# Kernel tuning notes

Hardware: AMD Instinct MI355X
Metric: run time of the kernel (lower is better)

The kernel has to match this reference:

```python
import jax, jax.numpy as jnp
import numpy as np

EPS = 0.01      # label smoothing eps
LAM = 0.5       # SuperLoss lam
ALPHA = 0.25    # FocalLoss alpha
GAMMA = 2.0     # FocalLoss gamma


def lambertw_principal(y, iters=20):
    """Real principal-branch Lambert W for y >= -1/e, via Halley iterations.
    Replaces the scipy.special.lambertw CPU round-trip with on-device math."""
    y = jnp.maximum(y, -jnp.exp(-1.0) + 1e-7)  # clamp to domain of W0
    # init: branch-point series near -1/e, log1p-based elsewhere
    p = jnp.sqrt(2.0 * (jnp.e * y + 1.0))
    w_bp = -1.0 + p - p * p / 3.0
    w = jnp.where(y < 0.0, w_bp, jnp.log1p(y))

    def body(w, _):
        ew = jnp.exp(w)
        f = w * ew - y
        w1 = w + 1.0
        w_next = w - f / (ew * w1 - (w + 2.0) * f / (2.0 * w1))
        return w_next, None

    w, _ = jax.lax.scan(body, w, None, length=iters)
    return w


def setup_inputs() -> dict:
    key = jax.random.key(0)
    k1, k2 = jax.random.split(key)
    B, C = 2048, 50257
    output = jax.random.normal(k1, (B, C), dtype=jnp.float32)
    target = jax.random.randint(k2, (B,), 0, C, dtype=jnp.int64)
    return {"output": output, "target": target}


def reference(output, target):
    B, c = output.shape
    # label-smoothing uniform term: mean over batch of -sum(log_softmax)
    log_preds = jax.nn.log_softmax(output, axis=-1)          # [B, C]
    loss = (-log_preds.sum(axis=-1)).mean()                  # scalar

    # FocalLoss(Superloss=True) applied to log_preds (CE re-applies log_softmax,
    # idempotent on log_preds but kept for fidelity)
    lp2 = jax.nn.log_softmax(log_preds, axis=-1)
    ce = -jnp.take_along_axis(lp2, target[:, None], axis=-1)[:, 0]  # [B]
    pt = jnp.exp(-ce)
    focal = ALPHA * (1.0 - pt) ** GAMMA * ce                 # [B]

    # SuperLoss: sigma computed from detached loss (stop_gradient)
    tau = jnp.log(jnp.float32(c))                            # C == classes
    l_det = jax.lax.stop_gradient(focal)
    cl_score = l_det - tau
    y_ = 0.5 * jnp.maximum(-2.0 / jnp.e, cl_score / LAM)
    sigma = jnp.exp(-lambertw_principal(y_))                 # [B]
    sl = (focal - tau) * sigma + LAM * jnp.log(sigma) ** 2
    sl_mean = sl.mean()

    loss_cls = loss * EPS / c + (1.0 - EPS) * sl_mean
    return loss_cls, jnp.exp(sl_mean)
```

## Files before the change

kernel.cpp:

```cpp
#include <hip/hip_runtime.h>
#include <hip/hip_bf16.h>
#include <math.h>


#define EPS_LS 0.01
#define LAM 0.5
#define ALPHA 0.25

__global__ __launch_bounds__(256) void
row_kernel(const float* __restrict__ x, const int* __restrict__ tgt,
           double* __restrict__ ws, int B, int C) {
    const int row = blockIdx.x;
    const int tid = threadIdx.x;
    const float* xr = x + (size_t)row * (size_t)C;

    float m  = -3.402823466e38f;
    float s  = 0.0f;
    float sx = 0.0f;

    const int mis = (int)(((size_t)row * (size_t)C) & 3);
    const int pre = (4 - mis) & 3;
    if (tid < pre) {
        float v = xr[tid];
        m = v; s = 1.0f; sx = v;
    }
    const int nvec = (C - pre) >> 2;
    const float4* xv = reinterpret_cast<const float4*>(xr + pre);
    for (int i = tid; i < nvec; i += 256) {
        float4 v = xv[i];
        float mx = fmaxf(fmaxf(v.x, v.y), fmaxf(v.z, v.w));
        float nm = fmaxf(m, mx);
        s = s * __expf(m - nm)
          + __expf(v.x - nm) + __expf(v.y - nm)
          + __expf(v.z - nm) + __expf(v.w - nm);
        m = nm;
        sx += (v.x + v.y) + (v.z + v.w);
    }
    const int done = pre + (nvec << 2);
    const int rem = C - done;
    if (tid < rem) {
        float v = xr[done + tid];
        float nm = fmaxf(m, v);
        s = s * __expf(m - nm) + __expf(v - nm);
        m = nm;
        sx += v;
    }

    for (int off = 32; off > 0; off >>= 1) {
        float mo  = __shfl_down(m, off, 64);
        float so  = __shfl_down(s, off, 64);
        float sxo = __shfl_down(sx, off, 64);
        float nm = fmaxf(m, mo);
        s = s * __expf(m - nm) + so * __expf(mo - nm);
        m = nm;
        sx += sxo;
    }

    __shared__ float sh_m[4], sh_s[4], sh_sx[4];
    const int wave = tid >> 6, lane = tid & 63;
    if (lane == 0) { sh_m[wave] = m; sh_s[wave] = s; sh_sx[wave] = sx; }
    __syncthreads();

    if (tid == 0) {
        float M = sh_m[0], S = sh_s[0], SX = sh_sx[0];
        for (int wv = 1; wv < 4; ++wv) {
            float nm = fmaxf(M, sh_m[wv]);
            S = S * __expf(M - nm) + sh_s[wv] * __expf(sh_m[wv] - nm);
            M = nm;
            SX += sh_sx[wv];
        }
        const double lse = log((double)S);
        const double xt  = (double)xr[tgt[row]];
        const double ce  = (double)M + lse - xt;
        const double pt  = exp(-ce);
        const double omp = 1.0 - pt;
        const double focal = ALPHA * omp * omp * ce;
        const double tau = log((double)C);
        const double cl  = focal - tau;
        const double Econst = 2.718281828459045235360287;
        double y_ = 0.5 * fmax(-2.0 / Econst, cl / LAM);
        double y  = fmax(y_, -exp(-1.0) + 1e-7);
        double p  = sqrt(2.0 * (Econst * y + 1.0));
        double w  = (y < 0.0) ? (-1.0 + p - p * p / 3.0) : log1p(y);
        for (int it = 0; it < 20; ++it) {
            double ew = exp(w);
            double f  = w * ew - y;
            double w1 = w + 1.0;
            w = w - f / (ew * w1 - (w + 2.0) * f / (2.0 * w1));
        }
        const double sigma = exp(-w);
        const double lw = log(sigma);
        const double sl = cl * sigma + LAM * lw * lw;
        const double rowloss = (double)C * ((double)M + lse) - (double)SX;
        ws[row]     = sl;
        ws[B + row] = rowloss;
    }
}

__global__ __launch_bounds__(256) void
finalize_kernel(const double* __restrict__ ws, float* __restrict__ out,
                int B, int C) {
    __shared__ double shA[256], shB[256];
    const int tid = threadIdx.x;
    double a = 0.0, b = 0.0;
    for (int i = tid; i < B; i += 256) {
        a += ws[i];
        b += ws[B + i];
    }
    shA[tid] = a; shB[tid] = b;
    __syncthreads();
    for (int off = 128; off > 0; off >>= 1) {
        if (tid < off) { shA[tid] += shA[tid + off]; shB[tid] += shB[tid + off]; }
        __syncthreads();
    }
    if (tid == 0) {
        const double sl_mean = shA[0] / (double)B;
        const double loss    = shB[0] / (double)B;
        const double loss_cls = loss * (EPS_LS / (double)C) + (1.0 - EPS_LS) * sl_mean;
        out[0] = (float)loss_cls;
        out[1] = (float)exp(sl_mean);
    }
}

extern "C" void kernel_launch(void* const* d_in, const int* in_sizes, int n_in,
                              void* d_out, int out_size, void* d_ws, size_t ws_size,
                              hipStream_t stream) {
    const float* x   = (const float*)d_in[0];
    const int*   tgt = (const int*)d_in[1];
    float* out = (float*)d_out;
    double* ws = (double*)d_ws;

    const int B = in_sizes[1];
    const int C = in_sizes[0] / B;

    row_kernel<<<B, 256, 0, stream>>>(x, tgt, ws, B, C);
    finalize_kernel<<<1, 256, 0, stream>>>(ws, out, B, C);
}
```

Baseline: 543.0 us.

## Unroll row scan with dual accumulators and nontemporal loads, move scalar math to finalize

The row kernel now issues two independent vector loads per iteration with nontemporal hints, keeps two online-softmax accumulators and merges them at the end. This is meant to raise memory-level parallelism and cut streaming cache pollution. The per-row double-precision focal and Lambert-W work moves from thread 0 of each row block into the single-block finalize kernel, which shortens the tail of each row block. The cost is that finalize now runs this serial double math for 8 rows per thread on one workgroup and gathers target logits from global memory.

```diff
diff --git a/kernel.cpp b/kernel.cpp
--- a/kernel.cpp
+++ b/kernel.cpp
@@ -7,77 +7,107 @@
 #define LAM 0.5
 #define ALPHA 0.25
 
+typedef float vf4 __attribute__((ext_vector_type(4)));
+
+struct Acc { float m, s, sx; };
+
+__device__ __forceinline__ void acc_vec(Acc& a, vf4 v) {
+    float mx = fmaxf(fmaxf(v.x, v.y), fmaxf(v.z, v.w));
+    float nm = fmaxf(a.m, mx);
+    a.s = a.s * __expf(a.m - nm)
+        + __expf(v.x - nm) + __expf(v.y - nm)
+        + __expf(v.z - nm) + __expf(v.w - nm);
+    a.m = nm;
+    a.sx += (v.x + v.y) + (v.z + v.w);
+}
+
+__device__ __forceinline__ void acc_merge(Acc& a, float mo, float so, float sxo) {
+    float nm = fmaxf(a.m, mo);
+    a.s = a.s * __expf(a.m - nm) + so * __expf(mo - nm);
+    a.m = nm;
+    a.sx += sxo;
+}
+
 __global__ __launch_bounds__(256) void
-row_kernel(const float* __restrict__ x, const int* __restrict__ tgt,
-           double* __restrict__ ws, int B, int C) {
+row_kernel(const float* __restrict__ x, float4* __restrict__ ws, int C) {
     const int row = blockIdx.x;
     const int tid = threadIdx.x;
     const float* xr = x + (size_t)row * (size_t)C;
 
-    float m  = -3.402823466e38f;
-    float s  = 0.0f;
-    float sx = 0.0f;
+    Acc a0 = { -3.402823466e38f, 0.0f, 0.0f };
+    Acc a1 = { -3.402823466e38f, 0.0f, 0.0f };
 
     const int mis = (int)(((size_t)row * (size_t)C) & 3);
     const int pre = (4 - mis) & 3;
     if (tid < pre) {
         float v = xr[tid];
-        m = v; s = 1.0f; sx = v;
+        a0.m = v; a0.s = 1.0f; a0.sx = v;
     }
     const int nvec = (C - pre) >> 2;
-    const float4* xv = reinterpret_cast<const float4*>(xr + pre);
-    for (int i = tid; i < nvec; i += 256) {
-        float4 v = xv[i];
-        float mx = fmaxf(fmaxf(v.x, v.y), fmaxf(v.z, v.w));
-        float nm = fmaxf(m, mx);
-        s = s * __expf(m - nm)
-          + __expf(v.x - nm) + __expf(v.y - nm)
-          + __expf(v.z - nm) + __expf(v.w - nm);
-        m = nm;
-        sx += (v.x + v.y) + (v.z + v.w);
+    const vf4* xv = reinterpret_cast<const vf4*>(xr + pre);
+
+    int i = tid;
+    for (; i + 256 < nvec; i += 512) {
+        vf4 v0 = __builtin_nontemporal_load(&xv[i]);
+        vf4 v1 = __builtin_nontemporal_load(&xv[i + 256]);
+        acc_vec(a0, v0);
+        acc_vec(a1, v1);
+    }
+    if (i < nvec) {
+        vf4 v0 = __builtin_nontemporal_load(&xv[i]);
+        acc_vec(a0, v0);
     }
     const int done = pre + (nvec << 2);
     const int rem = C - done;
     if (tid < rem) {
         float v = xr[done + tid];
-        float nm = fmaxf(m, v);
-        s = s * __expf(m - nm) + __expf(v - nm);
-        m = nm;
-        sx += v;
+        float nm = fmaxf(a0.m, v);
+        a0.s = a0.s * __expf(a0.m - nm) + __expf(v - nm);
+        a0.m = nm;
+        a0.sx += v;
     }
+    acc_merge(a0, a1.m, a1.s, a1.sx);
 
     for (int off = 32; off > 0; off >>= 1) {
-        float mo  = __shfl_down(m, off, 64);
-        float so  = __shfl_down(s, off, 64);
-        float sxo = __shfl_down(sx, off, 64);
-        float nm = fmaxf(m, mo);
-        s = s * __expf(m - nm) + so * __expf(mo - nm);
-        m = nm;
-        sx += sxo;
+        float mo  = __shfl_down(a0.m,  off, 64);
+        float so  = __shfl_down(a0.s,  off, 64);
+        float sxo = __shfl_down(a0.sx, off, 64);
+        acc_merge(a0, mo, so, sxo);
     }
 
     __shared__ float sh_m[4], sh_s[4], sh_sx[4];
     const int wave = tid >> 6, lane = tid & 63;
-    if (lane == 0) { sh_m[wave] = m; sh_s[wave] = s; sh_sx[wave] = sx; }
+    if (lane == 0) { sh_m[wave] = a0.m; sh_s[wave] = a0.s; sh_sx[wave] = a0.sx; }
     __syncthreads();
 
     if (tid == 0) {
-        float M = sh_m[0], S = sh_s[0], SX = sh_sx[0];
-        for (int wv = 1; wv < 4; ++wv) {
-            float nm = fmaxf(M, sh_m[wv]);
-            S = S * __expf(M - nm) + sh_s[wv] * __expf(sh_m[wv] - nm);
-            M = nm;
-            SX += sh_sx[wv];
-        }
-        const double lse = log((double)S);
-        const double xt  = (double)xr[tgt[row]];
-        const double ce  = (double)M + lse - xt;
-        const double pt  = exp(-ce);
+        Acc A = { sh_m[0], sh_s[0], sh_sx[0] };
+        for (int wv = 1; wv < 4; ++wv) acc_merge(A, sh_m[wv], sh_s[wv], sh_sx[wv]);
+        ws[row] = make_float4(A.m, A.s, A.sx, 0.0f);
+    }
+}
+
+__global__ __launch_bounds__(256) void
+finalize_kernel(const float4* __restrict__ ws, const float* __restrict__ x,
+                const int* __restrict__ tgt, float* __restrict__ out,
+                int B, int C) {
+    __shared__ double shA[256], shB[256];
+    const int tid = threadIdx.x;
+    const double tau = log((double)C);
+    const double Econst = 2.718281828459045235360287;
+
+    double sl_sum = 0.0, loss_sum = 0.0;
+    for (int row = tid; row < B; row += 256) {
+        float4 r = ws[row];
+        const double M = (double)r.x;
+        const double lse = log((double)r.y);
+        const double SX = (double)r.z;
+        const double xt = (double)x[(size_t)row * (size_t)C + tgt[row]];
+        const double ce = M + lse - xt;
+        const double pt = exp(-ce);
         const double omp = 1.0 - pt;
         const double focal = ALPHA * omp * omp * ce;
-        const double tau = log((double)C);
-        const double cl  = focal - tau;
-        const double Econst = 2.718281828459045235360287;
+        const double cl = focal - tau;
         double y_ = 0.5 * fmax(-2.0 / Econst, cl / LAM);
         double y  = fmax(y_, -exp(-1.0) + 1e-7);
         double p  = sqrt(2.0 * (Econst * y + 1.0));
@@ -90,24 +120,10 @@
         }
         const double sigma = exp(-w);
         const double lw = log(sigma);
-        const double sl = cl * sigma + LAM * lw * lw;
-        const double rowloss = (double)C * ((double)M + lse) - (double)SX;
-        ws[row]     = sl;
-        ws[B + row] = rowloss;
+        sl_sum   += cl * sigma + LAM * lw * lw;
+        loss_sum += (double)C * (M + lse) - SX;
     }
-}
-
-__global__ __launch_bounds__(256) void
-finalize_kernel(const double* __restrict__ ws, float* __restrict__ out,
-                int B, int C) {
-    __shared__ double shA[256], shB[256];
-    const int tid = threadIdx.x;
-    double a = 0.0, b = 0.0;
-    for (int i = tid; i < B; i += 256) {
-        a += ws[i];
-        b += ws[B + i];
-    }
-    shA[tid] = a; shB[tid] = b;
+    shA[tid] = sl_sum; shB[tid] = loss_sum;
     __syncthreads();
     for (int off = 128; off > 0; off >>= 1) {
         if (tid < off) { shA[tid] += shA[tid + off]; shB[tid] += shB[tid + off]; }
@@ -128,11 +144,11 @@
     const float* x   = (const float*)d_in[0];
     const int*   tgt = (const int*)d_in[1];
     float* out = (float*)d_out;
-    double* ws = (double*)d_ws;
+    float4* ws = (float4*)d_ws;
 
     const int B = in_sizes[1];
     const int C = in_sizes[0] / B;
 
-    row_kernel<<<B, 256, 0, stream>>>(x, tgt, ws, B, C);
-    finalize_kernel<<<1, 256, 0, stream>>>(ws, out, B, C);
+    row_kernel<<<B, 256, 0, stream>>>(x, ws, C);
+    finalize_kernel<<<1, 256, 0, stream>>>(ws, x, tgt, out, B, C);
 }
```

After: 535.0 us. No clear change (-1.5%).
